# Kernel optimization log

Measured on AMD Instinct MI355X. Metric: run time of the kernel, lower is better.

The kernel has to match this reference:

```python
import jax, jax.numpy as jnp
import numpy as np

B, L, TOPK, NUM_RBF, NUM_POS, MAX_REL, CH = 4, 1024, 30, 16, 16, 32, 128
EDGE_IN = NUM_POS + NUM_RBF * 25 + 18  # 434
NODE_IN = 22


def _normalize(x, axis=-1):
    n = jnp.linalg.norm(x, axis=axis, keepdims=True)
    return jnp.where(n > 0, x / jnp.where(n > 0, n, 1.0), 0.0)


def layer_norm(x, g, b, eps=1e-5):
    mu = jnp.mean(x, axis=-1, keepdims=True)
    var = jnp.var(x, axis=-1, keepdims=True)
    return (x - mu) / jnp.sqrt(var + eps) * g + b


def gather_nodes_d(nodes, idx):
    # nodes [B,M,C], idx [B,N,K] -> [B,N,K,C]
    Bn, N, K = idx.shape
    out = jnp.take_along_axis(nodes, idx.reshape(Bn, N * K, 1), axis=1)
    return out.reshape(Bn, N, K, nodes.shape[-1])


def gather_edges(edges, idx):
    # edges [B,N,N,C], idx [B,N,K] -> [B,N,K,C]
    return jnp.take_along_axis(edges, idx[..., None], axis=2)


def cal_dihedral(Xf, eps=1e-7):
    U = _normalize(Xf[:, 1:, :] - Xf[:, :-1, :])
    u_0, u_1, u_2 = U[:, :-2], U[:, 1:-1], U[:, 2:]
    n_0 = _normalize(jnp.cross(u_0, u_1))
    n_1 = _normalize(jnp.cross(u_1, u_2))
    cosD = jnp.clip(jnp.sum(n_0 * n_1, -1), -1 + eps, 1 - eps)
    v = _normalize(jnp.cross(n_0, n_1))
    return jnp.sign(jnp.sum(-v * u_1, -1)) * jnp.arccos(cosD)


def _dihedrals(X, eps=1e-7):
    Bn, N = X.shape[0], X.shape[1]
    Xf = X[:, :, :3, :].reshape(Bn, 3 * N, 3)
    D = jnp.pad(cal_dihedral(Xf), ((0, 0), (1, 2))).reshape(Bn, N, 3)
    dihedral_feats = jnp.concatenate([jnp.cos(D), jnp.sin(D)], -1)
    U = _normalize(Xf[:, 1:, :] - Xf[:, :-1, :])
    cosA = jnp.clip(jnp.sum(U[:, :-2] * U[:, 1:-1], -1), -1 + eps, 1 - eps)
    A = jnp.pad(jnp.arccos(cosA), ((0, 0), (1, 2))).reshape(Bn, N, 3)
    angle_feats = jnp.concatenate([jnp.cos(A), jnp.sin(A)], -1)
    return jnp.concatenate([dihedral_feats, angle_feats], -1)  # [B,N,12]


def _quaternions(R):
    diag = jnp.diagonal(R, axis1=-2, axis2=-1)
    Rxx, Ryy, Rzz = diag[..., 0], diag[..., 1], diag[..., 2]
    mags = 0.5 * jnp.sqrt(jnp.abs(1.0 + jnp.stack([Rxx - Ryy - Rzz, -Rxx + Ryy - Rzz, -Rxx - Ryy + Rzz], -1)))
    signs = jnp.sign(jnp.stack([R[..., 2, 1] - R[..., 1, 2], R[..., 0, 2] - R[..., 2, 0], R[..., 1, 0] - R[..., 0, 1]], -1))
    w = jnp.sqrt(jax.nn.relu(1.0 + jnp.sum(diag, -1, keepdims=True))) / 2.0
    return _normalize(jnp.concatenate([signs * mags, w], -1))


def _orientations_coarse_gl_tuple(X, E_idx):
    V = X  # [B,N,4,3]
    Bn, N = X.shape[0], X.shape[1]
    Xf = X[:, :, :3, :].reshape(Bn, 3 * N, 3)
    U = _normalize(Xf[:, 1:, :] - Xf[:, :-1, :])
    u_0, u_1 = U[:, :-2], U[:, 1:-1]
    n_0 = _normalize(jnp.cross(u_0, u_1))[:, ::3]  # [B,N-1,3]
    b_1 = _normalize(u_0 - u_1)[:, ::3]
    Xa = Xf[:, ::3]  # N-atom coords [B,N,3]
    Q = jnp.stack([b_1, n_0, jnp.cross(b_1, n_0)], 2).reshape(Bn, N - 1, 9)
    Q = jnp.pad(Q, ((0, 0), (0, 1), (0, 0)))  # [B,N,9]
    Qm = Q.reshape(Bn, N, 3, 3)
    Q_neighbors = gather_nodes_d(Q, E_idx).reshape(Bn, N, -1, 3, 3)
    X_nb = gather_nodes_d(V[:, :, 1, :], E_idx)
    N_nb = gather_nodes_d(V[:, :, 0, :], E_idx)
    C_nb = gather_nodes_d(V[:, :, 2, :], E_idx)
    O_nb = gather_nodes_d(V[:, :, 3, :], E_idx)
    dXn = jnp.stack([X_nb, N_nb, C_nb, O_nb], 3) - Xa[:, :, None, None, :]  # [B,N,K,4,3]
    dU = jnp.einsum('bnij,bnkaj->bnkai', Qm, dXn)
    Kn = E_idx.shape[-1]
    E_direct = _normalize(dU).reshape(Bn, N, Kn, 12)
    R = jnp.einsum('bnji,bnkjl->bnkil', Qm, Q_neighbors)
    q = _quaternions(R)  # [B,N,K,4]
    dX_inner = V[:, :, jnp.array([0, 2, 3]), :] - Xa[:, :, None, :]
    V_direct = _normalize(jnp.einsum('bnij,bnaj->bnai', Qm, dX_inner)).reshape(Bn, N, 9)
    return V_direct, E_direct, q


def _dist(Xc, mask, eps=1e-6):
    mask_2D = mask[:, None, :] * mask[:, :, None]
    D = mask_2D * jnp.sqrt(jnp.sum((Xc[:, None, :, :] - Xc[:, :, None, :]) ** 2, -1) + eps)
    D_max = jnp.max(D, -1, keepdims=True)
    D_adjust = D + (1.0 - mask_2D) * D_max
    negD, E_idx = jax.lax.top_k(-D_adjust, min(TOPK, Xc.shape[1]))
    return -negD, E_idx


def _dist_seq(res_idx):
    D = jnp.abs(res_idx[:, :, None] - res_idx[:, None, :])
    _, E_idx = jax.lax.top_k(-D, min(TOPK, res_idx.shape[1]))
    return E_idx


def _rbf(D):
    D_mu = jnp.linspace(2.0, 22.0, NUM_RBF)
    D_sigma = (22.0 - 2.0) / NUM_RBF
    return jnp.exp(-(((D[..., None] - D_mu) / D_sigma) ** 2))


def _get_rbf(A, Bm, E_idx):
    D = jnp.sqrt(jnp.sum((A[:, :, None, :] - Bm[:, None, :, :]) ** 2, -1) + 1e-6)
    return _rbf(gather_edges(D[..., None], E_idx)[..., 0])


PAIRS = [('N', 'N'), ('C', 'C'), ('O', 'O'), ('Cb', 'Cb'), ('Ca', 'N'), ('Ca', 'C'), ('Ca', 'O'), ('Ca', 'Cb'),
         ('N', 'C'), ('N', 'O'), ('N', 'Cb'), ('Cb', 'C'), ('Cb', 'O'), ('O', 'C'), ('N', 'Ca'), ('C', 'Ca'),
         ('O', 'Ca'), ('Cb', 'Ca'), ('C', 'N'), ('O', 'N'), ('Cb', 'N'), ('C', 'Cb'), ('O', 'Cb'), ('C', 'O')]


def _forward(X, mask, residue_idx, chain_labels, W_pos, b_pos, W_edge, W_node, g_edge, b_edge, g_node, b_node):
    bvec = X[:, :, 1, :] - X[:, :, 0, :]
    cvec = X[:, :, 2, :] - X[:, :, 1, :]
    avec = jnp.cross(bvec, cvec)
    Cb = -0.58273431 * avec + 0.56802827 * bvec - 0.54067466 * cvec + X[:, :, 1, :]
    atoms = {'N': X[:, :, 0, :], 'Ca': X[:, :, 1, :], 'C': X[:, :, 2, :], 'O': X[:, :, 3, :], 'Cb': Cb}
    D_neighbors, E_idx = _dist(atoms['Ca'], mask)
    E_idx_res = _dist_seq(residue_idx)
    E_idx = jnp.where(mask[:, :, None] == 0, E_idx_res, E_idx)
    RBF_all = [_rbf(D_neighbors)]
    for pa, pb in PAIRS:
        RBF_all.append(_get_rbf(atoms[pa], atoms[pb], E_idx))
    RBF_all = jnp.concatenate(RBF_all, -1)  # [B,L,K,400]
    V_angles = _dihedrals(X) * mask[..., None]
    V_direct, E_direct, E_angles = _orientations_coarse_gl_tuple(X, E_idx)
    V_direct = V_direct * mask[..., None]
    offset = residue_idx[:, :, None] - residue_idx[:, None, :]
    E_offset = gather_edges(offset[..., None], E_idx)[..., 0]
    d_chains = (chain_labels[:, :, None] == chain_labels[:, None, :]).astype(jnp.int32)
    E_chains = gather_edges(d_chains[..., None], E_idx)[..., 0]
    d = jnp.clip(E_offset + MAX_REL, 0, 2 * MAX_REL) * E_chains + (1 - E_chains) * (2 * MAX_REL + 1)
    E_positional = jax.nn.one_hot(d, 2 * MAX_REL + 2, dtype=W_pos.dtype) @ W_pos + b_pos
    mask_j = gather_nodes_d(mask[..., None], E_idx)[..., 0]
    fdt = E_direct.dtype
    E = jnp.concatenate([E_positional, RBF_all, E_direct, E_angles,
                         E_chains[..., None].astype(fdt), mask_j[..., None]], -1)  # [B,L,K,434]
    E = layer_norm(E @ W_edge, g_edge, b_edge)
    Vn = jnp.concatenate([V_angles, V_direct, mask[..., None]], -1)  # [B,L,22]
    Vn = layer_norm(Vn @ W_node, g_node, b_node)
    return Vn, E, E_idx


def setup_inputs():
    key = jax.random.key(0)
    ks = jax.random.split(key, 8)
    X = 3.0 * jax.random.normal(ks[0], (B, L, 4, 3), jnp.float32)
    mask = jnp.ones((B, L), jnp.float32)
    residue_idx = jnp.tile(jnp.arange(L, dtype=jnp.int32), (B, 1))
    chain_labels = jax.random.randint(ks[1], (B, L), 0, 2, dtype=jnp.int32)
    s = lambda k, sh: jax.random.normal(k, sh, jnp.float32) * 0.05
    W_pos = s(ks[2], (2 * MAX_REL + 2, NUM_POS))
    b_pos = jnp.zeros((NUM_POS,), jnp.float32)
    W_edge = s(ks[3], (EDGE_IN, CH))
    W_node = s(ks[4], (NODE_IN, CH))
    return dict(X=X, mask=mask, residue_idx=residue_idx, chain_labels=chain_labels,
                W_pos=W_pos, b_pos=b_pos, W_edge=W_edge, W_node=W_node,
                g_edge=jnp.ones((CH,), jnp.float32), b_edge=jnp.zeros((CH,), jnp.float32),
                g_node=jnp.ones((CH,), jnp.float32), b_node=jnp.zeros((CH,), jnp.float32))


def reference(X, mask, residue_idx, chain_labels, W_pos, b_pos, W_edge, W_node, g_edge, b_edge, g_node, b_node):
    return _forward(X, mask, residue_idx, chain_labels, W_pos, b_pos, W_edge, W_node,
                    g_edge, b_edge, g_node, b_node)
```

## Files before the change

kernel.cpp:

```cpp
#include <hip/hip_runtime.h>

#define BATCH 4
#define LEN   1024
#define KNB   30
#define CH    128
#define EIN   434
#define KP    448
#define KST   14
#define ASTR  456
#define CSTR  132

typedef unsigned short ushort_t;
typedef __attribute__((ext_vector_type(8))) short bf16x8;
typedef __attribute__((ext_vector_type(4))) float f32x4;

__constant__ int c_pa[24] = {0,2,3,4,1,1,1,1,0,0,0,4,4,3,0,2,3,4,2,3,4,2,3,2};
__constant__ int c_pb[24] = {0,2,3,4,0,2,3,4,2,3,4,2,3,2,1,1,1,1,0,0,0,4,4,3};

struct F3 { float x, y, z; };
__device__ __forceinline__ F3 f3sub(F3 a, F3 b){ return {a.x-b.x, a.y-b.y, a.z-b.z}; }
__device__ __forceinline__ F3 f3cross(F3 a, F3 b){
  return {a.y*b.z - a.z*b.y, a.z*b.x - a.x*b.z, a.x*b.y - a.y*b.x};
}
__device__ __forceinline__ float f3dot(F3 a, F3 b){ return a.x*b.x + a.y*b.y + a.z*b.z; }
__device__ __forceinline__ F3 f3norm(F3 a){
  float n = sqrtf(f3dot(a,a));
  if (n > 0.f) return {a.x/n, a.y/n, a.z/n};
  return {0.f, 0.f, 0.f};
}
__device__ __forceinline__ float fsign(float x){ return (x > 0.f) ? 1.f : ((x < 0.f) ? -1.f : 0.f); }
__device__ __forceinline__ float clip1(float c){ return fminf(fmaxf(c, -1.f + 1e-7f), 1.f - 1e-7f); }
__device__ __forceinline__ float dihedralf(F3 ua, F3 ub, F3 uc){
  F3 n0 = f3norm(f3cross(ua, ub));
  F3 n1 = f3norm(f3cross(ub, uc));
  float cd = clip1(f3dot(n0, n1));
  F3 v = f3norm(f3cross(n0, n1));
  return fsign(-f3dot(v, ub)) * acosf(cd);
}
__device__ __forceinline__ ushort_t f2bf(float f){
  unsigned u = __float_as_uint(f);
  unsigned r = u + 0x7FFFu + ((u >> 16) & 1u);
  return (ushort_t)(r >> 16);
}

#define DPP_MIN_STEP(v, ctrl) do{                                            \
    unsigned t_ = (unsigned)__builtin_amdgcn_update_dpp(                     \
        (int)0xFFFFFFFF, (int)(v), (ctrl), 0xF, 0xF, false);                 \
    (v) = t_ < (v) ? t_ : (v);                                               \
  } while(0)
__device__ __forceinline__ unsigned wave_min_u32(unsigned v){
  DPP_MIN_STEP(v, 0x111);
  DPP_MIN_STEP(v, 0x112);
  DPP_MIN_STEP(v, 0x114);
  DPP_MIN_STEP(v, 0x118);
  DPP_MIN_STEP(v, 0x142);
  DPP_MIN_STEP(v, 0x143);
  return (unsigned)__builtin_amdgcn_readlane((int)v, 63);
}

__global__ __launch_bounds__(256) void prep_kernel(
    const float* __restrict__ X, const float* __restrict__ mask,
    const float* __restrict__ We,
    float* __restrict__ wCb, float* __restrict__ wQ, float* __restrict__ wVn,
    float* __restrict__ wCa, ushort_t* __restrict__ Wfrag)
{
  if (blockIdx.x >= 16){
    int f = (blockIdx.x - 16)*256 + threadIdx.x;
    if (f >= 8*KST*64) return;
    int t = f / (KST*64);
    int s = (f / 64) % KST;
    int l = f & 63;
    int n  = t*16 + (l & 15);
    int k0 = s*32 + (l >> 4)*8;
    ushort_t v[8];
    #pragma unroll
    for (int j = 0; j < 8; ++j){
      int k = k0 + j;
      v[j] = (k < EIN) ? f2bf(We[(size_t)k*CH + n]) : (ushort_t)0;
    }
    ulong2* dst = (ulong2*)(Wfrag + (size_t)f*8);
    *dst = *(ulong2*)v;
    return;
  }

  int idx = blockIdx.x * 256 + threadIdx.x;
  int n = idx & (LEN - 1);
  const float* p = X + (size_t)idx * 12;
  F3 Na = {p[0], p[1], p[2]};
  F3 Ca = {p[3], p[4], p[5]};
  F3 Cc = {p[6], p[7], p[8]};
  F3 Oa = {p[9], p[10], p[11]};
  wCa[idx*4+0] = Ca.x; wCa[idx*4+1] = Ca.y; wCa[idx*4+2] = Ca.z; wCa[idx*4+3] = 0.f;
  F3 bv = f3sub(Ca, Na);
  F3 cv = f3sub(Cc, Ca);
  F3 av = f3cross(bv, cv);
  wCb[idx*3+0] = -0.58273431f*av.x + 0.56802827f*bv.x - 0.54067466f*cv.x + Ca.x;
  wCb[idx*3+1] = -0.58273431f*av.y + 0.56802827f*bv.y - 0.54067466f*cv.y + Ca.y;
  wCb[idx*3+2] = -0.58273431f*av.z + 0.56802827f*bv.z - 0.54067466f*cv.z + Ca.z;

  F3 u0 = f3norm(bv);
  F3 u1 = f3norm(cv);

  float Q[9];
  if (n < LEN - 1){
    F3 b1 = f3norm(f3sub(u0, u1));
    F3 n0 = f3norm(f3cross(u0, u1));
    F3 r2 = f3cross(b1, n0);
    Q[0]=b1.x; Q[1]=b1.y; Q[2]=b1.z;
    Q[3]=n0.x; Q[4]=n0.y; Q[5]=n0.z;
    Q[6]=r2.x; Q[7]=r2.y; Q[8]=r2.z;
  } else {
    #pragma unroll
    for (int t = 0; t < 9; ++t) Q[t] = 0.f;
  }
  #pragma unroll
  for (int t = 0; t < 9; ++t) wQ[(size_t)idx*9 + t] = Q[t];

  float m = mask[idx];
  bool hp = (n > 0), hn = (n < LEN - 1);
  F3 um1 = {0,0,0}, u2 = {0,0,0}, u3 = {0,0,0};
  if (hp){
    const float* pp = p - 12;
    F3 Cp = {pp[6], pp[7], pp[8]};
    um1 = f3norm(f3sub(Na, Cp));
  }
  if (hn){
    const float* pn = p + 12;
    F3 Nn  = {pn[0], pn[1], pn[2]};
    F3 Can = {pn[3], pn[4], pn[5]};
    u2 = f3norm(f3sub(Nn, Cc));
    u3 = f3norm(f3sub(Can, Nn));
  }
  float D0=0.f, D1=0.f, D2=0.f, A0=0.f, A1=0.f, A2=0.f;
  if (hp){ D0 = dihedralf(um1, u0, u1); A0 = acosf(clip1(f3dot(um1, u0))); }
  if (hn){
    D1 = dihedralf(u0, u1, u2); A1 = acosf(clip1(f3dot(u0, u1)));
    D2 = dihedralf(u1, u2, u3); A2 = acosf(clip1(f3dot(u1, u2)));
  }
  float vn[22];
  vn[0] = cosf(D0)*m; vn[1] = cosf(D1)*m; vn[2]  = cosf(D2)*m;
  vn[3] = sinf(D0)*m; vn[4] = sinf(D1)*m; vn[5]  = sinf(D2)*m;
  vn[6] = cosf(A0)*m; vn[7] = cosf(A1)*m; vn[8]  = cosf(A2)*m;
  vn[9] = sinf(A0)*m; vn[10]= sinf(A1)*m; vn[11] = sinf(A2)*m;
  F3 dxs[3];
  dxs[0] = {0.f, 0.f, 0.f};
  dxs[1] = f3sub(Cc, Na);
  dxs[2] = f3sub(Oa, Na);
  #pragma unroll
  for (int a = 0; a < 3; ++a){
    F3 dv = dxs[a];
    F3 du = { Q[0]*dv.x + Q[1]*dv.y + Q[2]*dv.z,
              Q[3]*dv.x + Q[4]*dv.y + Q[5]*dv.z,
              Q[6]*dv.x + Q[7]*dv.y + Q[8]*dv.z };
    F3 dn = f3norm(du);
    vn[12 + a*3 + 0] = dn.x * m;
    vn[12 + a*3 + 1] = dn.y * m;
    vn[12 + a*3 + 2] = dn.z * m;
  }
  vn[21] = m;
  #pragma unroll
  for (int t = 0; t < 22; ++t) wVn[(size_t)idx*22 + t] = vn[t];
}

__global__ __launch_bounds__(256) void topk_kernel(
    const float* __restrict__ wCa, float* __restrict__ wDn,
    int* __restrict__ wIdx, float* __restrict__ outI)
{
  int wid = threadIdx.x >> 6, l = threadIdx.x & 63;
  int bi = blockIdx.x*4 + wid;
  int b  = bi >> 10;
  const float4* Ca = (const float4*)wCa;
  float4 ci = Ca[bi];
  const float4* Cb = Ca + (size_t)b * LEN;

  unsigned D[16];
  #pragma unroll
  for (int t = 0; t < 16; ++t){
    int j = l + 64*t;
    float4 cj = Cb[j];
    float dx = ci.x - cj.x, dy = ci.y - cj.y, dz = ci.z - cj.z;
    D[t] = __float_as_uint(sqrtf(dx*dx + dy*dy + dz*dz + 1e-6f));
  }
  unsigned lmin = D[0]; unsigned jmin = (unsigned)l;
  #pragma unroll
  for (int t = 1; t < 16; ++t)
    if (D[t] < lmin){ lmin = D[t]; jmin = (unsigned)(l + 64*t); }

  for (int k = 0; k < KNB; ++k){
    unsigned dmin = wave_min_u32(lmin);
    unsigned cand = (lmin == dmin) ? jmin : 0xFFFFFFFFu;
    unsigned jwin = wave_min_u32(cand);
    if (cand == jwin){
      wIdx[bi*KNB + k] = (int)jwin;
      wDn[bi*KNB + k]  = __uint_as_float(dmin);
      outI[bi*KNB + k] = (float)jwin;
      int tw = (int)(jwin >> 6);
      #pragma unroll
      for (int t = 0; t < 16; ++t) if (t == tw) D[t] = 0xFFFFFFFFu;
      lmin = D[0]; jmin = (unsigned)l;
      #pragma unroll
      for (int t = 1; t < 16; ++t)
        if (D[t] < lmin){ lmin = D[t]; jmin = (unsigned)(l + 64*t); }
    }
  }
}

__global__ __launch_bounds__(64) void node_kernel(
    const float* __restrict__ wVn, const float* __restrict__ Wn,
    const float* __restrict__ gn, const float* __restrict__ bn,
    float* __restrict__ outV)
{
  int bi = blockIdx.x;
  int t  = threadIdx.x;
  __shared__ float v[22];
  if (t < 22) v[t] = wVn[(size_t)bi*22 + t];
  __syncthreads();
  float x0 = 0.f, x1 = 0.f;
  #pragma unroll
  for (int r = 0; r < 22; ++r){
    float vr = v[r];
    x0 = fmaf(vr, Wn[r*CH + t], x0);
    x1 = fmaf(vr, Wn[r*CH + t + 64], x1);
  }
  float s = x0 + x1;
  #pragma unroll
  for (int off = 1; off < 64; off <<= 1) s += __shfl_xor(s, off);
  float mu = s * (1.f/128.f);
  float d0 = x0 - mu, d1 = x1 - mu;
  float vs = d0*d0 + d1*d1;
  #pragma unroll
  for (int off = 1; off < 64; off <<= 1) vs += __shfl_xor(vs, off);
  float inv = 1.f / sqrtf(vs * (1.f/128.f) + 1e-5f);
  outV[(size_t)bi*CH + t]      = d0*inv*gn[t]    + bn[t];
  outV[(size_t)bi*CH + t + 64] = d1*inv*gn[t+64] + bn[t+64];
}

__global__ __launch_bounds__(256) void edge_kernel(
    const float* __restrict__ X, const float* __restrict__ mask,
    const int* __restrict__ resi, const int* __restrict__ chain,
    const float* __restrict__ Wp, const float* __restrict__ bp,
    const float* __restrict__ ge, const float* __restrict__ be,
    const float* __restrict__ wCb, const float* __restrict__ wQ,
    const float* __restrict__ wDn, const int* __restrict__ wIdx,
    const ushort_t* __restrict__ Wfrag,
    float* __restrict__ outE)
{
  __shared__ __align__(16) ushort_t As[32*ASTR];
  __shared__ float sAI[15];
  __shared__ float sQi[9];
  __shared__ float sAJ[KNB][15];
  __shared__ float sQj[KNB][9];
  __shared__ int   sOffI[KNB];
  __shared__ float sChain[KNB];
  __shared__ float sMaskJ[KNB];
  __shared__ float sDn[KNB];

  int bi  = blockIdx.x;
  int b   = bi >> 10;
  int tid = threadIdx.x;

  if (tid < KNB){
    int j  = wIdx[bi*KNB + tid];
    int gj = (b << 10) + j;
    const float* pj = X + (size_t)gj * 12;
    #pragma unroll
    for (int t = 0; t < 12; ++t) sAJ[tid][t] = pj[t];
    sAJ[tid][12] = wCb[(size_t)gj*3 + 0];
    sAJ[tid][13] = wCb[(size_t)gj*3 + 1];
    sAJ[tid][14] = wCb[(size_t)gj*3 + 2];
    #pragma unroll
    for (int t = 0; t < 9; ++t) sQj[tid][t] = wQ[(size_t)gj*9 + t];
    sOffI[tid]  = resi[bi] - resi[gj];
    sChain[tid] = (chain[bi] == chain[gj]) ? 1.f : 0.f;
    sMaskJ[tid] = mask[gj];
    sDn[tid]    = wDn[bi*KNB + tid];
  } else if (tid == KNB){
    const float* pi = X + (size_t)bi * 12;
    #pragma unroll
    for (int t = 0; t < 12; ++t) sAI[t] = pi[t];
    sAI[12] = wCb[(size_t)bi*3 + 0];
    sAI[13] = wCb[(size_t)bi*3 + 1];
    sAI[14] = wCb[(size_t)bi*3 + 2];
  } else if (tid == KNB + 1){
    #pragma unroll
    for (int t = 0; t < 9; ++t) sQi[t] = wQ[(size_t)bi*9 + t];
  }
  for (int e = tid; e < 2*KP; e += 256) As[30*ASTR + (e >= KP ? ASTR + e - KP : e)] = 0;
  for (int e = tid; e < KNB*14; e += 256){
    int r = e / 14, c = EIN + (e % 14);
    As[r*ASTR + c] = 0;
  }
  __syncthreads();

  if (tid < KNB*8){
    int k = tid >> 3, s = tid & 7;
    ushort_t* row = &As[k*ASTR];
    if (s == 0){
      int off = sOffI[k];
      float ch = sChain[k];
      int d = off + 32;
      d = d < 0 ? 0 : (d > 64 ? 64 : d);
      if (!(ch > 0.5f)) d = 65;
      #pragma unroll
      for (int m2 = 0; m2 < 16; ++m2)
        row[m2] = f2bf(Wp[d*16 + m2] + bp[m2]);
      row[432] = f2bf(ch);
      row[433] = f2bf(sMaskJ[k]);
    } else if (s == 1){
      float nx = sAI[0], ny = sAI[1], nz = sAI[2];
      const int amap[4] = {3, 0, 6, 9};
      #pragma unroll
      for (int a = 0; a < 4; ++a){
        float dx = sAJ[k][amap[a]+0] - nx;
        float dy = sAJ[k][amap[a]+1] - ny;
        float dz = sAJ[k][amap[a]+2] - nz;
        float e0 = sQi[0]*dx + sQi[1]*dy + sQi[2]*dz;
        float e1 = sQi[3]*dx + sQi[4]*dy + sQi[5]*dz;
        float e2 = sQi[6]*dx + sQi[7]*dy + sQi[8]*dz;
        float nn = sqrtf(e0*e0 + e1*e1 + e2*e2);
        float inv = nn > 0.f ? 1.f/nn : 0.f;
        row[416 + a*3 + 0] = f2bf(e0*inv);
        row[416 + a*3 + 1] = f2bf(e1*inv);
        row[416 + a*3 + 2] = f2bf(e2*inv);
      }
    } else if (s == 2){
      float R[3][3];
      #pragma unroll
      for (int i2 = 0; i2 < 3; ++i2)
        #pragma unroll
        for (int l2 = 0; l2 < 3; ++l2)
          R[i2][l2] = sQi[0*3+i2]*sQj[k][0*3+l2]
                    + sQi[1*3+i2]*sQj[k][1*3+l2]
                    + sQi[2*3+i2]*sQj[k][2*3+l2];
      float Rxx = R[0][0], Ryy = R[1][1], Rzz = R[2][2];
      float mx = 0.5f*sqrtf(fabsf(1.f + Rxx - Ryy - Rzz));
      float my = 0.5f*sqrtf(fabsf(1.f - Rxx + Ryy - Rzz));
      float mz = 0.5f*sqrtf(fabsf(1.f - Rxx - Ryy + Rzz));
      float qx = fsign(R[2][1] - R[1][2]) * mx;
      float qy = fsign(R[0][2] - R[2][0]) * my;
      float qz = fsign(R[1][0] - R[0][1]) * mz;
      float qw = sqrtf(fmaxf(1.f + Rxx + Ryy + Rzz, 0.f)) * 0.5f;
      float qn = sqrtf(qx*qx + qy*qy + qz*qz + qw*qw);
      float inv = qn > 0.f ? 1.f/qn : 0.f;
      row[428] = f2bf(qx*inv);
      row[429] = f2bf(qy*inv);
      row[430] = f2bf(qz*inv);
      row[431] = f2bf(qw*inv);
    }
    for (int p = s; p < 25; p += 8){
      float d;
      if (p == 0) d = sDn[k];
      else {
        int ai = c_pa[p-1]*3, bj = c_pb[p-1]*3;
        float dx = sAI[ai+0] - sAJ[k][bj+0];
        float dy = sAI[ai+1] - sAJ[k][bj+1];
        float dz = sAI[ai+2] - sAJ[k][bj+2];
        d = sqrtf(dx*dx + dy*dy + dz*dz + 1e-6f);
      }
      #pragma unroll
      for (int m2 = 0; m2 < 16; ++m2){
        float mu = (float)(2.0 + m2 * (20.0/15.0));
        float tt = (d - mu) * 0.8f;
        row[16 + p*16 + m2] = f2bf(__expf(-tt*tt));
      }
    }
  }
  __syncthreads();

  int w = tid >> 6, l = tid & 63;
  int n0 = w*2;
  int aOff0 = (l & 15)*ASTR + (l >> 4)*8;
  int aOff1 = aOff0 + 16*ASTR;
  const ushort_t* bp0 = Wfrag + ((size_t)(n0    *KST)*64 + l)*8;
  const ushort_t* bp1 = Wfrag + ((size_t)((n0+1)*KST)*64 + l)*8;

  f32x4 acc00 = {0.f,0.f,0.f,0.f}, acc01 = acc00, acc10 = acc00, acc11 = acc00;

  bf16x8 a0 = *(const bf16x8*)&As[aOff0];
  bf16x8 a1 = *(const bf16x8*)&As[aOff1];
  bf16x8 b0 = *(const bf16x8*)bp0;
  bf16x8 b1 = *(const bf16x8*)bp1;
  #pragma unroll
  for (int s = 0; s < KST; ++s){
    bf16x8 a0n, a1n, b0n, b1n;
    if (s < KST-1){
      int ka = (s+1)*32;
      a0n = *(const bf16x8*)&As[aOff0 + ka];
      a1n = *(const bf16x8*)&As[aOff1 + ka];
      b0n = *(const bf16x8*)(bp0 + (size_t)(s+1)*64*8);
      b1n = *(const bf16x8*)(bp1 + (size_t)(s+1)*64*8);
    }
    acc00 = __builtin_amdgcn_mfma_f32_16x16x32_bf16(a0, b0, acc00, 0, 0, 0);
    acc01 = __builtin_amdgcn_mfma_f32_16x16x32_bf16(a0, b1, acc01, 0, 0, 0);
    acc10 = __builtin_amdgcn_mfma_f32_16x16x32_bf16(a1, b0, acc10, 0, 0, 0);
    acc11 = __builtin_amdgcn_mfma_f32_16x16x32_bf16(a1, b1, acc11, 0, 0, 0);
    if (s < KST-1){ a0 = a0n; a1 = a1n; b0 = b0n; b1 = b1n; }
  }
  __syncthreads();

  float* Cs = (float*)As;
  int ccol = l & 15, crow = (l >> 4)*4;
  #pragma unroll
  for (int r = 0; r < 4; ++r){
    Cs[(crow + r)*CSTR      + n0*16 + ccol]      = acc00[r];
    Cs[(crow + r)*CSTR      + (n0+1)*16 + ccol]  = acc01[r];
    Cs[(16 + crow + r)*CSTR + n0*16 + ccol]      = acc10[r];
    Cs[(16 + crow + r)*CSTR + (n0+1)*16 + ccol]  = acc11[r];
  }
  __syncthreads();

  if (tid < KNB*8){
    int row = tid >> 3, g = tid & 7;
    float v[16];
    #pragma unroll
    for (int c = 0; c < 16; ++c) v[c] = Cs[row*CSTR + g*16 + c];
    float s = 0.f;
    #pragma unroll
    for (int c = 0; c < 16; ++c) s += v[c];
    #pragma unroll
    for (int off = 1; off < 8; off <<= 1) s += __shfl_xor(s, off, 8);
    float mu = s * (1.f/128.f);
    float vs = 0.f;
    #pragma unroll
    for (int c = 0; c < 16; ++c){ float dd = v[c] - mu; vs += dd*dd; }
    #pragma unroll
    for (int off = 1; off < 8; off <<= 1) vs += __shfl_xor(vs, off, 8);
    float inv = 1.f / sqrtf(vs * (1.f/128.f) + 1e-5f);
    float o[16];
    #pragma unroll
    for (int c = 0; c < 16; ++c)
      o[c] = (v[c] - mu)*inv*ge[g*16 + c] + be[g*16 + c];
    float4* dst = (float4*)&outE[((size_t)bi*KNB + row)*CH + g*16];
    dst[0] = make_float4(o[0], o[1], o[2], o[3]);
    dst[1] = make_float4(o[4], o[5], o[6], o[7]);
    dst[2] = make_float4(o[8], o[9], o[10], o[11]);
    dst[3] = make_float4(o[12], o[13], o[14], o[15]);
  }
}

extern "C" void kernel_launch(void* const* d_in, const int* in_sizes, int n_in,
                              void* d_out, int out_size, void* d_ws, size_t ws_size,
                              hipStream_t stream)
{
  const float* X    = (const float*)d_in[0];
  const float* mask = (const float*)d_in[1];
  const int*   resi = (const int*)  d_in[2];
  const int*   chn  = (const int*)  d_in[3];
  const float* Wp   = (const float*)d_in[4];
  const float* bp   = (const float*)d_in[5];
  const float* We   = (const float*)d_in[6];
  const float* Wn   = (const float*)d_in[7];
  const float* ge   = (const float*)d_in[8];
  const float* be   = (const float*)d_in[9];
  const float* gn   = (const float*)d_in[10];
  const float* bn   = (const float*)d_in[11];

  float* outV = (float*)d_out;
  float* outE = outV + (size_t)BATCH*LEN*CH;
  float* outI = outE + (size_t)BATCH*LEN*KNB*CH;

  float* ws   = (float*)d_ws;
  float* wCb  = ws;
  float* wQ   = wCb + (size_t)BATCH*LEN*3;
  float* wVn  = wQ  + (size_t)BATCH*LEN*9;
  float* wDn  = wVn + (size_t)BATCH*LEN*22;
  int*   wIdx = (int*)(wDn + (size_t)BATCH*LEN*KNB);
  float* wCa  = (float*)(wIdx + (size_t)BATCH*LEN*KNB);
  ushort_t* Wfrag = (ushort_t*)(wCa + (size_t)BATCH*LEN*4);

  prep_kernel<<<16 + 28, 256, 0, stream>>>(X, mask, We, wCb, wQ, wVn, wCa, Wfrag);
  topk_kernel<<<BATCH*LEN/4, 256, 0, stream>>>(wCa, wDn, wIdx, outI);
  node_kernel<<<BATCH*LEN, 64, 0, stream>>>(wVn, Wn, gn, bn, outV);
  edge_kernel<<<BATCH*LEN, 256, 0, stream>>>(X, mask, resi, chn, Wp, bp, ge, be,
                                             wCb, wQ, wDn, wIdx, Wfrag, outE);
}
```

Measured before the change: 187.7 us.

## Fuse node embedding into edge kernel and vectorize bf16 shared-memory writes

Removes the separate node_kernel launch and computes the node linear plus layernorm in the last 16 threads of the edge kernel, which are idle during the edge layernorm epilogue. Feature writes into the shared A tile now pack pairs of floats to bf16 and store them with 64/128-bit writes instead of scalar ushort stores. Padding zeroing and epilogue reads are vectorized too. The new pack helper rounds half-up instead of to nearest even, which can differ slightly in the last bit.

```diff
diff --git a/kernel.cpp b/kernel.cpp
--- a/kernel.cpp
+++ b/kernel.cpp
@@ -41,6 +41,11 @@
   unsigned u = __float_as_uint(f);
   unsigned r = u + 0x7FFFu + ((u >> 16) & 1u);
   return (ushort_t)(r >> 16);
+}
+__device__ __forceinline__ unsigned pk2(float a, float b){
+  unsigned ua = (__float_as_uint(a) + 0x8000u) >> 16;
+  unsigned ub = (__float_as_uint(b) + 0x8000u) & 0xFFFF0000u;
+  return ua | ub;
 }
 
 #define DPP_MIN_STEP(v, ctrl) do{                                            \
@@ -205,49 +210,23 @@
   }
 }
 
-__global__ __launch_bounds__(64) void node_kernel(
-    const float* __restrict__ wVn, const float* __restrict__ Wn,
-    const float* __restrict__ gn, const float* __restrict__ bn,
-    float* __restrict__ outV)
-{
-  int bi = blockIdx.x;
-  int t  = threadIdx.x;
-  __shared__ float v[22];
-  if (t < 22) v[t] = wVn[(size_t)bi*22 + t];
-  __syncthreads();
-  float x0 = 0.f, x1 = 0.f;
-  #pragma unroll
-  for (int r = 0; r < 22; ++r){
-    float vr = v[r];
-    x0 = fmaf(vr, Wn[r*CH + t], x0);
-    x1 = fmaf(vr, Wn[r*CH + t + 64], x1);
-  }
-  float s = x0 + x1;
-  #pragma unroll
-  for (int off = 1; off < 64; off <<= 1) s += __shfl_xor(s, off);
-  float mu = s * (1.f/128.f);
-  float d0 = x0 - mu, d1 = x1 - mu;
-  float vs = d0*d0 + d1*d1;
-  #pragma unroll
-  for (int off = 1; off < 64; off <<= 1) vs += __shfl_xor(vs, off);
-  float inv = 1.f / sqrtf(vs * (1.f/128.f) + 1e-5f);
-  outV[(size_t)bi*CH + t]      = d0*inv*gn[t]    + bn[t];
-  outV[(size_t)bi*CH + t + 64] = d1*inv*gn[t+64] + bn[t+64];
-}
-
 __global__ __launch_bounds__(256) void edge_kernel(
     const float* __restrict__ X, const float* __restrict__ mask,
     const int* __restrict__ resi, const int* __restrict__ chain,
     const float* __restrict__ Wp, const float* __restrict__ bp,
     const float* __restrict__ ge, const float* __restrict__ be,
+    const float* __restrict__ Wn, const float* __restrict__ gn,
+    const float* __restrict__ bn,
     const float* __restrict__ wCb, const float* __restrict__ wQ,
+    const float* __restrict__ wVn,
     const float* __restrict__ wDn, const int* __restrict__ wIdx,
     const ushort_t* __restrict__ Wfrag,
-    float* __restrict__ outE)
+    float* __restrict__ outV, float* __restrict__ outE)
 {
   __shared__ __align__(16) ushort_t As[32*ASTR];
   __shared__ float sAI[15];
   __shared__ float sQi[9];
+  __shared__ float sVn[22];
   __shared__ float sAJ[KNB][15];
   __shared__ float sQj[KNB][9];
   __shared__ int   sOffI[KNB];
@@ -284,11 +263,18 @@
   } else if (tid == KNB + 1){
     #pragma unroll
     for (int t = 0; t < 9; ++t) sQi[t] = wQ[(size_t)bi*9 + t];
-  }
-  for (int e = tid; e < 2*KP; e += 256) As[30*ASTR + (e >= KP ? ASTR + e - KP : e)] = 0;
-  for (int e = tid; e < KNB*14; e += 256){
-    int r = e / 14, c = EIN + (e % 14);
-    As[r*ASTR + c] = 0;
+  } else if (tid >= 32 && tid < 54){
+    sVn[tid - 32] = wVn[(size_t)bi*22 + (tid - 32)];
+  } else if (tid >= 64 && tid < 176){
+    int idx = tid - 64;
+    int r = 30 + (idx / 56), c8 = idx % 56;
+    *(uint4*)&As[r*ASTR + c8*8] = make_uint4(0,0,0,0);
+  } else if (tid >= 176 && tid < 176 + KNB){
+    int r = tid - 176;
+    ushort_t* row = &As[r*ASTR];
+    *(unsigned*)&row[434] = 0u;
+    *(uint2*)&row[436] = make_uint2(0,0);
+    *(uint4*)&row[440] = make_uint4(0,0,0,0);
   }
   __syncthreads();
 
@@ -301,14 +287,22 @@
       int d = off + 32;
       d = d < 0 ? 0 : (d > 64 ? 64 : d);
       if (!(ch > 0.5f)) d = 65;
+      const float4* wp4 = (const float4*)(Wp + d*16);
+      const float4* bp4 = (const float4*)bp;
+      float e[16];
       #pragma unroll
-      for (int m2 = 0; m2 < 16; ++m2)
-        row[m2] = f2bf(Wp[d*16 + m2] + bp[m2]);
-      row[432] = f2bf(ch);
-      row[433] = f2bf(sMaskJ[k]);
+      for (int q = 0; q < 4; ++q){
+        float4 wv = wp4[q], bv = bp4[q];
+        e[q*4+0] = wv.x + bv.x; e[q*4+1] = wv.y + bv.y;
+        e[q*4+2] = wv.z + bv.z; e[q*4+3] = wv.w + bv.w;
+      }
+      *(uint4*)&row[0] = make_uint4(pk2(e[0],e[1]), pk2(e[2],e[3]), pk2(e[4],e[5]), pk2(e[6],e[7]));
+      *(uint4*)&row[8] = make_uint4(pk2(e[8],e[9]), pk2(e[10],e[11]), pk2(e[12],e[13]), pk2(e[14],e[15]));
+      *(unsigned*)&row[432] = pk2(ch, sMaskJ[k]);
     } else if (s == 1){
       float nx = sAI[0], ny = sAI[1], nz = sAI[2];
       const int amap[4] = {3, 0, 6, 9};
+      float e[12];
       #pragma unroll
       for (int a = 0; a < 4; ++a){
         float dx = sAJ[k][amap[a]+0] - nx;
@@ -319,10 +313,10 @@
         float e2 = sQi[6]*dx + sQi[7]*dy + sQi[8]*dz;
         float nn = sqrtf(e0*e0 + e1*e1 + e2*e2);
         float inv = nn > 0.f ? 1.f/nn : 0.f;
-        row[416 + a*3 + 0] = f2bf(e0*inv);
-        row[416 + a*3 + 1] = f2bf(e1*inv);
-        row[416 + a*3 + 2] = f2bf(e2*inv);
+        e[a*3+0] = e0*inv; e[a*3+1] = e1*inv; e[a*3+2] = e2*inv;
       }
+      *(uint4*)&row[416] = make_uint4(pk2(e[0],e[1]), pk2(e[2],e[3]), pk2(e[4],e[5]), pk2(e[6],e[7]));
+      *(uint2*)&row[424] = make_uint2(pk2(e[8],e[9]), pk2(e[10],e[11]));
     } else if (s == 2){
       float R[3][3];
       #pragma unroll
@@ -342,10 +336,7 @@
       float qw = sqrtf(fmaxf(1.f + Rxx + Ryy + Rzz, 0.f)) * 0.5f;
       float qn = sqrtf(qx*qx + qy*qy + qz*qz + qw*qw);
       float inv = qn > 0.f ? 1.f/qn : 0.f;
-      row[428] = f2bf(qx*inv);
-      row[429] = f2bf(qy*inv);
-      row[430] = f2bf(qz*inv);
-      row[431] = f2bf(qw*inv);
+      *(uint2*)&row[428] = make_uint2(pk2(qx*inv, qy*inv), pk2(qz*inv, qw*inv));
     }
     for (int p = s; p < 25; p += 8){
       float d;
@@ -357,12 +348,15 @@
         float dz = sAI[ai+2] - sAJ[k][bj+2];
         d = sqrtf(dx*dx + dy*dy + dz*dz + 1e-6f);
       }
+      float e[16];
       #pragma unroll
       for (int m2 = 0; m2 < 16; ++m2){
         float mu = (float)(2.0 + m2 * (20.0/15.0));
         float tt = (d - mu) * 0.8f;
-        row[16 + p*16 + m2] = f2bf(__expf(-tt*tt));
+        e[m2] = __expf(-tt*tt);
       }
+      *(uint4*)&row[16 + p*16]     = make_uint4(pk2(e[0],e[1]), pk2(e[2],e[3]), pk2(e[4],e[5]), pk2(e[6],e[7]));
+      *(uint4*)&row[16 + p*16 + 8] = make_uint4(pk2(e[8],e[9]), pk2(e[10],e[11]), pk2(e[12],e[13]), pk2(e[14],e[15]));
     }
   }
   __syncthreads();
@@ -411,9 +405,10 @@
 
   if (tid < KNB*8){
     int row = tid >> 3, g = tid & 7;
-    float v[16];
-    #pragma unroll
-    for (int c = 0; c < 16; ++c) v[c] = Cs[row*CSTR + g*16 + c];
+    const float4* src = (const float4*)&Cs[row*CSTR + g*16];
+    float4 v0 = src[0], v1 = src[1], v2 = src[2], v3 = src[3];
+    float v[16] = {v0.x,v0.y,v0.z,v0.w, v1.x,v1.y,v1.z,v1.w,
+                   v2.x,v2.y,v2.z,v2.w, v3.x,v3.y,v3.z,v3.w};
     float s = 0.f;
     #pragma unroll
     for (int c = 0; c < 16; ++c) s += v[c];
@@ -435,6 +430,38 @@
     dst[1] = make_float4(o[4], o[5], o[6], o[7]);
     dst[2] = make_float4(o[8], o[9], o[10], o[11]);
     dst[3] = make_float4(o[12], o[13], o[14], o[15]);
+  } else if (tid >= 240){
+    int c0 = (tid - 240)*8;
+    float x[8] = {0,0,0,0,0,0,0,0};
+    #pragma unroll
+    for (int r = 0; r < 22; ++r){
+      float vr = sVn[r];
+      float4 w0 = *(const float4*)&Wn[r*CH + c0];
+      float4 w1 = *(const float4*)&Wn[r*CH + c0 + 4];
+      x[0] = fmaf(vr, w0.x, x[0]); x[1] = fmaf(vr, w0.y, x[1]);
+      x[2] = fmaf(vr, w0.z, x[2]); x[3] = fmaf(vr, w0.w, x[3]);
+      x[4] = fmaf(vr, w1.x, x[4]); x[5] = fmaf(vr, w1.y, x[5]);
+      x[6] = fmaf(vr, w1.z, x[6]); x[7] = fmaf(vr, w1.w, x[7]);
+    }
+    float s = 0.f;
+    #pragma unroll
+    for (int c = 0; c < 8; ++c) s += x[c];
+    #pragma unroll
+    for (int off = 1; off < 16; off <<= 1) s += __shfl_xor(s, off, 16);
+    float mu = s * (1.f/128.f);
+    float vs = 0.f;
+    #pragma unroll
+    for (int c = 0; c < 8; ++c){ float dd = x[c] - mu; vs += dd*dd; }
+    #pragma unroll
+    for (int off = 1; off < 16; off <<= 1) vs += __shfl_xor(vs, off, 16);
+    float inv = 1.f / sqrtf(vs * (1.f/128.f) + 1e-5f);
+    float o[8];
+    #pragma unroll
+    for (int c = 0; c < 8; ++c)
+      o[c] = (x[c] - mu)*inv*gn[c0 + c] + bn[c0 + c];
+    float4* dst = (float4*)&outV[(size_t)bi*CH + c0];
+    dst[0] = make_float4(o[0], o[1], o[2], o[3]);
+    dst[1] = make_float4(o[4], o[5], o[6], o[7]);
   }
 }
 
@@ -470,7 +497,7 @@
 
   prep_kernel<<<16 + 28, 256, 0, stream>>>(X, mask, We, wCb, wQ, wVn, wCa, Wfrag);
   topk_kernel<<<BATCH*LEN/4, 256, 0, stream>>>(wCa, wDn, wIdx, outI);
-  node_kernel<<<BATCH*LEN, 64, 0, stream>>>(wVn, Wn, gn, bn, outV);
   edge_kernel<<<BATCH*LEN, 256, 0, stream>>>(X, mask, resi, chn, Wp, bp, ge, be,
-                                             wCb, wQ, wDn, wIdx, Wfrag, outE);
-}
+                                             Wn, gn, bn, wCb, wQ, wVn,
+                                             wDn, wIdx, Wfrag, outV, outE);
+}
```

Measured after the change: 193.9 us. 1.03x slower.
